# Kernel optimization log

Hardware: AMD Instinct MI355X
Metric: run time of the kernel (lower is better)

Reference implementation:

```python
import jax, jax.numpy as jnp
import numpy as np
import math

H = 4096; NH = 32; QLR = 1536; KVLR = 512
DN = 128; DR = 64; DV = 128; QD = DN + DR  # q_head_dim = 192
B = 1; S = 2048
BASE = 50000.0; FACTOR = 32.0; ORIG_MAX = 4096; BETA_FAST = 32.0; BETA_SLOW = 1.0
EPS = 1e-6
_M = 0.1 * 1.0 * math.log(FACTOR) + 1.0  # yarn mscale (mscale_all_dim=1)
SCALE = (QD ** -0.5) * _M * _M


def _yarn_cos_sin(seq_len):
    dim = DR
    f = np.arange(0, dim, 2, dtype=np.float32) / dim
    freq_extra = 1.0 / BASE ** f
    freq_inter = 1.0 / (FACTOR * BASE ** f)
    def corr(nr):
        return dim * math.log(ORIG_MAX / (nr * 2 * math.pi)) / (2 * math.log(BASE))
    low = max(math.floor(corr(BETA_FAST)), 0)
    high = min(math.ceil(corr(BETA_SLOW)), dim - 1)
    hi = high + 0.001 if low == high else float(high)
    ramp = np.clip((np.arange(dim // 2, dtype=np.float32) - low) / (hi - low), 0.0, 1.0)
    inv_freq_mask = 1.0 - ramp
    inv_freq = freq_inter * (1.0 - inv_freq_mask) + freq_extra * inv_freq_mask
    t = np.arange(seq_len, dtype=np.float32)
    fr = np.outer(t, inv_freq)
    emb = np.concatenate([fr, fr], axis=-1)
    # mscale ratio = get_mscale(f,1)/get_mscale(f,1) = 1.0
    return jnp.asarray(np.cos(emb)), jnp.asarray(np.sin(emb))


def _rms(x, w):
    v = jnp.mean(x.astype(jnp.float32) ** 2, axis=-1, keepdims=True)
    return w * (x.astype(jnp.float32) * jax.lax.rsqrt(v + EPS)).astype(x.dtype)


def _reorder(x):
    # interleaved -> [evens, odds] (matches view(d//2,2).transpose.reshape)
    d = x.shape[-1]
    x = x.reshape(x.shape[:-1] + (d // 2, 2))
    return jnp.concatenate([x[..., 0], x[..., 1]], axis=-1)


def _rotate_half(x):
    h = x.shape[-1] // 2
    return jnp.concatenate([-x[..., h:], x[..., :h]], axis=-1)


def _rope(x, cos, sin):
    x = _reorder(x)
    return x * cos + _rotate_half(x) * sin


def setup_inputs() -> dict:
    key = jax.random.key(0)
    ks = jax.random.split(key, 6)
    hs = jax.random.normal(ks[0], (B, S, H), dtype=jnp.float32)
    causal = jnp.tril(jnp.ones((S, S), dtype=bool))
    mask = jnp.where(causal, 0.0, -1e9).astype(jnp.float32)[None, None]
    pos = jnp.broadcast_to(jnp.arange(S, dtype=jnp.int64 if jax.config.jax_enable_x64 else jnp.int32), (B, S))
    def w(k, shape, fan_in):
        return jax.random.normal(k, shape, dtype=jnp.float32) * (fan_in ** -0.5)
    return {
        "hidden_states": hs,
        "attention_mask": mask,
        "position_ids": pos,
        "q_a_w": w(ks[1], (QLR, H), H),
        "q_a_ln_w": jnp.ones((QLR,), jnp.float32),
        "q_b_w": w(ks[2], (NH * QD, QLR), QLR),
        "kv_a_w": w(ks[3], (KVLR + DR, H), H),
        "kv_a_ln_w": jnp.ones((KVLR,), jnp.float32),
        "kv_b_w": w(ks[4], (NH * (DN + DV), KVLR), KVLR),
        "o_w": w(ks[5], (H, NH * DV), NH * DV),
    }


def reference(hidden_states, attention_mask, position_ids, q_a_w, q_a_ln_w, q_b_w, kv_a_w, kv_a_ln_w, kv_b_w, o_w):
    b, s, _ = hidden_states.shape
    q = _rms(hidden_states @ q_a_w.T, q_a_ln_w) @ q_b_w.T
    q = q.reshape(b, s, NH, QD).transpose(0, 2, 1, 3)          # [b,h,s,192]
    q_nope, q_pe = q[..., :DN], q[..., DN:]
    ckv = hidden_states @ kv_a_w.T                              # [b,s,576]
    comp, k_pe = ckv[..., :KVLR], ckv[..., KVLR:]
    k_pe = k_pe.reshape(b, s, 1, DR).transpose(0, 2, 1, 3)      # [b,1,s,64]
    kv = (_rms(comp, kv_a_ln_w) @ kv_b_w.T).reshape(b, s, NH, DN + DV).transpose(0, 2, 1, 3)
    k_nope, v = kv[..., :DN], kv[..., DN:]
    cos, sin = _yarn_cos_sin(s)
    cos = cos[position_ids][:, None]                            # [b,1,s,64]
    sin = sin[position_ids][:, None]
    q_pe = _rope(q_pe, cos, sin)
    k_pe = _rope(k_pe, cos, sin)
    qs = jnp.concatenate([q_nope, q_pe], axis=-1)               # [b,h,s,192]
    ks = jnp.concatenate([k_nope, jnp.broadcast_to(k_pe, (b, NH, s, DR))], axis=-1)
    aw = jnp.einsum('bhqd,bhkd->bhqk', qs, ks) * SCALE
    aw = jax.nn.softmax((aw + attention_mask).astype(jnp.float32), axis=-1).astype(hidden_states.dtype)
    out = jnp.einsum('bhqk,bhkd->bhqd', aw, v)                  # [b,h,s,128]
    out = out.transpose(0, 2, 1, 3).reshape(b, s, NH * DV)
    return out @ o_w.T
```

## Files before the change

kernel.cpp:

```cpp
#include <hip/hip_runtime.h>
#include <hip/hip_fp16.h>

typedef _Float16 f16x8 __attribute__((ext_vector_type(8)));
typedef float f32x4 __attribute__((ext_vector_type(4)));

#define DEV __device__ __forceinline__

typedef const __attribute__((address_space(1))) void gvoid_t;
typedef __attribute__((address_space(3))) void lvoid_t;

DEV void gload16(const void* g, void* l) {
  __builtin_amdgcn_global_load_lds((gvoid_t*)g, (lvoid_t*)l, 16, 0, 0);
}

DEV f32x4 mfma16(f16x8 a, f16x8 b, f32x4 c) {
  return __builtin_amdgcn_mfma_f32_16x16x32_f16(a, b, c, 0, 0, 0);
}

__global__ __launch_bounds__(256) void cvt_kernel(const float* __restrict__ s,
                                                  __half* __restrict__ d, int n4) {
  int stride = gridDim.x * 256;
  for (int i = blockIdx.x * 256 + threadIdx.x; i < n4; i += stride) {
    float4 v = ((const float4*)s)[i];
    __align__(8) __half a[4] = {__float2half(v.x), __float2half(v.y),
                                __float2half(v.z), __float2half(v.w)};
    *((uint2*)(d + (size_t)i * 4)) = *((uint2*)a);
  }
}

__global__ __launch_bounds__(256) void cvt5_kernel(const float* __restrict__ s0,
                                                   const float* __restrict__ s1,
                                                   const float* __restrict__ s2,
                                                   const float* __restrict__ s3,
                                                   const float* __restrict__ s4,
                                                   __half* __restrict__ d0, __half* __restrict__ d1,
                                                   __half* __restrict__ d2, __half* __restrict__ d3,
                                                   __half* __restrict__ d4) {
  const int c0 = 2097152, c1 = 3670016, c2 = 4259840, c3 = 6619136, c4 = 7667712;
  int stride = gridDim.x * 256;
  for (int i = blockIdx.x * 256 + threadIdx.x; i < c4; i += stride) {
    const float* s;
    __half* d;
    int j;
    if (i < c0) { s = s0; d = d0; j = i; }
    else if (i < c1) { s = s1; d = d1; j = i - c0; }
    else if (i < c2) { s = s2; d = d2; j = i - c1; }
    else if (i < c3) { s = s3; d = d3; j = i - c2; }
    else { s = s4; d = d4; j = i - c3; }
    float4 v = ((const float4*)s)[j];
    __align__(8) __half a[4] = {__float2half(v.x), __float2half(v.y),
                                __float2half(v.z), __float2half(v.w)};
    *((uint2*)(d + (size_t)j * 4)) = *((uint2*)a);
  }
}

__global__ __launch_bounds__(256) void norm_rope_kernel(const float* __restrict__ qab,
                                                        const float* __restrict__ q_ln,
                                                        const float* __restrict__ kv_ln,
                                                        const float2* __restrict__ cs,
                                                        __half* __restrict__ qa_r,
                                                        __half* __restrict__ kv_r,
                                                        __half* __restrict__ Kb) {
  const int row = blockIdx.x, tid = threadIdx.x;
  const float* xr = qab + (size_t)row * 2112;
  float4 a0 = ((const float4*)xr)[tid];
  float4 a1 = make_float4(0.f, 0.f, 0.f, 0.f);
  float4 b0 = make_float4(0.f, 0.f, 0.f, 0.f);
  if (tid < 128) {
    a1 = ((const float4*)xr)[256 + tid];
    b0 = ((const float4*)(xr + 1536))[tid];
  }
  float sq = a0.x * a0.x + a0.y * a0.y + a0.z * a0.z + a0.w * a0.w +
             a1.x * a1.x + a1.y * a1.y + a1.z * a1.z + a1.w * a1.w;
  float sk = b0.x * b0.x + b0.y * b0.y + b0.z * b0.z + b0.w * b0.w;
  for (int mm = 1; mm <= 32; mm <<= 1) {
    sq += __shfl_xor(sq, mm);
    sk += __shfl_xor(sk, mm);
  }
  __shared__ float r1[4], r2[4];
  __shared__ __half ro[64];
  if ((tid & 63) == 0) { r1[tid >> 6] = sq; r2[tid >> 6] = sk; }
  if (tid < 32) {
    float x0 = xr[2048 + 2 * tid], x1 = xr[2048 + 2 * tid + 1];
    float2 c = cs[row * 32 + tid];
    ro[tid] = __float2half(x0 * c.x - x1 * c.y);
    ro[32 + tid] = __float2half(x1 * c.x + x0 * c.y);
  }
  __syncthreads();
  float rsq = rsqrtf((r1[0] + r1[1] + r1[2] + r1[3]) * (1.f / 1536.f) + 1e-6f);
  float rsk = rsqrtf((r2[0] + r2[1] + r2[2] + r2[3]) * (1.f / 512.f) + 1e-6f);
  __half* yq = qa_r + (size_t)row * 1536;
  {
    int j = tid * 4;
    yq[j + 0] = __float2half(q_ln[j + 0] * a0.x * rsq);
    yq[j + 1] = __float2half(q_ln[j + 1] * a0.y * rsq);
    yq[j + 2] = __float2half(q_ln[j + 2] * a0.z * rsq);
    yq[j + 3] = __float2half(q_ln[j + 3] * a0.w * rsq);
  }
  if (tid < 128) {
    int j = 1024 + tid * 4;
    yq[j + 0] = __float2half(q_ln[j + 0] * a1.x * rsq);
    yq[j + 1] = __float2half(q_ln[j + 1] * a1.y * rsq);
    yq[j + 2] = __float2half(q_ln[j + 2] * a1.z * rsq);
    yq[j + 3] = __float2half(q_ln[j + 3] * a1.w * rsq);
    __half* yk = kv_r + (size_t)row * 512;
    int jk = tid * 4;
    yk[jk + 0] = __float2half(kv_ln[jk + 0] * b0.x * rsk);
    yk[jk + 1] = __float2half(kv_ln[jk + 1] * b0.y * rsk);
    yk[jk + 2] = __float2half(kv_ln[jk + 2] * b0.z * rsk);
    yk[jk + 3] = __float2half(kv_ln[jk + 3] * b0.w * rsk);
  }
#pragma unroll
  for (int it = 0; it < 8; ++it) {
    int i = it * 256 + tid;
    int hh = i >> 6, d = i & 63;
    Kb[((size_t)hh * 2048 + row) * 192 + 128 + d] = ro[d];
  }
}

__global__ __launch_bounds__(256) void rope_table_kernel(const int* __restrict__ pos,
                                                         float2* __restrict__ cs) {
  int i = blockIdx.x * 256 + threadIdx.x;
  int row = i >> 5, j = i & 31;
  double f = (double)j * (1.0 / 32.0);
  double fe = exp(-f * 10.81977828441028);
  double fi = fe * (1.0 / 32.0);
  double ramp = fmin(fmax(((double)j - 8.0) * (1.0 / 12.0), 0.0), 1.0);
  double inv = fi * ramp + fe * (1.0 - ramp);
  double ang = (double)pos[row] * inv;
  cs[i] = make_float2((float)cos(ang), (float)sin(ang));
}

__global__ __launch_bounds__(256) void rope_q_kernel(const __half* __restrict__ qpe,
                                                     const float2* __restrict__ cs,
                                                     __half* __restrict__ Qb, float qscale) {
  int i = blockIdx.x * 256 + threadIdx.x;
  int row = i >> 10, rem = i & 1023, h = rem >> 5, j = rem & 31;
  float x0 = __half2float(qpe[(size_t)row * 2048 + h * 64 + 2 * j]);
  float x1 = __half2float(qpe[(size_t)row * 2048 + h * 64 + 2 * j + 1]);
  float2 c = cs[row * 32 + j];
  float o0 = (x0 * c.x - x1 * c.y) * qscale;
  float o1 = (x1 * c.x + x0 * c.y) * qscale;
  __half* dst = Qb + ((size_t)h * 2048 + row) * 192;
  dst[128 + j] = __float2half(o0);
  dst[160 + j] = __float2half(o1);
}

template <int BN, int EPI>
__global__ __launch_bounds__(256) void gemm128(const __half* __restrict__ A, int lda,
                                               const __half* __restrict__ B, int K, int Ncols,
                                               float* __restrict__ Cf, int ldc,
                                               __half* __restrict__ O1, __half* __restrict__ O2,
                                               float qscale) {
  constexpr int NFR = BN / 32;
  __shared__ __align__(16) char As[2 * 128 * 128];
  __shared__ __align__(16) char Bs[2 * BN * 128];
  const int tid = threadIdx.x;
  const int lane = tid & 63, w = tid >> 6;
  const int l15 = lane & 15, g = lane >> 4;
  const int wr = w >> 1, wc = w & 1;
  const int nwg = gridDim.x * gridDim.y;
  int wg = blockIdx.y * gridDim.x + blockIdx.x;
  wg = (wg & 7) * (nwg >> 3) + (wg >> 3);
  const int m0 = (wg / gridDim.x) * 128, n0 = (wg % gridDim.x) * BN;
  const int srow = lane >> 3;
  const int scol = ((lane & 7) ^ srow) * 8;
  f32x4 acc[4][NFR] = {};
  const int nt = K >> 6;

  auto stage = [&](int t, int buf) {
    const __half* Ab = A + t * 64 + scol;
    const __half* Bb = B + t * 64 + scol;
#pragma unroll
    for (int cc = 0; cc < 4; ++cc) {
      int ch = w * 4 + cc;
      gload16(Ab + (size_t)(m0 + ch * 8 + srow) * lda, As + buf * 16384 + ch * 1024);
    }
#pragma unroll
    for (int cc = 0; cc < NFR; ++cc) {
      int ch = w * NFR + cc;
      gload16(Bb + (size_t)(n0 + ch * 8 + srow) * K, Bs + buf * (BN * 128) + ch * 1024);
    }
  };

  stage(0, 0);
  __syncthreads();

  for (int t = 0; t < nt; ++t) {
    const int buf = t & 1;
    if (t + 1 < nt) stage(t + 1, buf ^ 1);
    const char* Ab = As + buf * 16384;
    const char* Bb = Bs + buf * (BN * 128);
#pragma unroll
    for (int kk = 0; kk < 2; ++kk) {
      f16x8 af[4], bf[NFR];
#pragma unroll
      for (int m = 0; m < 4; ++m) {
        int r = wr * 64 + m * 16 + l15;
        af[m] = *(const f16x8*)(Ab + r * 128 + (((kk << 2) | g) ^ (r & 7)) * 16);
      }
#pragma unroll
      for (int n = 0; n < NFR; ++n) {
        int r = wc * (BN / 2) + n * 16 + l15;
        bf[n] = *(const f16x8*)(Bb + r * 128 + (((kk << 2) | g) ^ (r & 7)) * 16);
      }
#pragma unroll
      for (int m = 0; m < 4; ++m)
#pragma unroll
        for (int n = 0; n < NFR; ++n) acc[m][n] = mfma16(af[m], bf[n], acc[m][n]);
    }
    __syncthreads();
  }

#pragma unroll
  for (int m = 0; m < 4; ++m)
#pragma unroll
    for (int n = 0; n < NFR; ++n)
#pragma unroll
      for (int i = 0; i < 4; ++i) {
        int row = m0 + wr * 64 + m * 16 + g * 4 + i;
        int col = n0 + wc * (BN / 2) + n * 16 + l15;
        float v = acc[m][n][i];
        if (EPI == 0) {
          if (col < Ncols) Cf[(size_t)row * ldc + col] = v;
        } else if (EPI == 2) {
          int h = col / 192, d = col - h * 192;
          if (d < 128)
            O1[((size_t)h * 2048 + row) * 192 + d] = __float2half(v * qscale);
          else
            O2[(size_t)row * 2048 + h * 64 + (d - 128)] = __float2half(v);
        } else if (EPI == 3) {
          int h = col >> 8, d = col & 255;
          if (d < 128)
            O1[((size_t)h * 2048 + row) * 192 + d] = __float2half(v);
          else
            O2[((size_t)h * 128 + (d - 128)) * 2048 + row] = __float2half(v);
        }
      }
}

__global__ __launch_bounds__(256) void attn_kernel(const __half* __restrict__ Q,
                                                   const __half* __restrict__ K,
                                                   const __half* __restrict__ Vt,
                                                   __half* __restrict__ Out) {
  __shared__ __align__(16) char Klds[2 * 64 * 384];
  __shared__ __align__(16) char Vlds[144 * 128];
  __shared__ __align__(16) __half Plds[4][16][72];
  int wg = blockIdx.y * gridDim.x + blockIdx.x;
  wg = (wg & 7) * 64 + (wg >> 3);
  const int pr = wg & 15, h = wg >> 4;
  const int tid = threadIdx.x, lane = tid & 63, w = tid >> 6;
  const int l15 = lane & 15, g = lane >> 4;

  const char* Kg = (const char*)(K + (size_t)h * 2048 * 192);
  const char* Vg = (const char*)(Vt + (size_t)h * 128 * 2048);

  if (tid < 128) {
    ((uint4*)(Vlds + 16384))[tid] =
        make_uint4(0x3C003C00u, 0x3C003C00u, 0x3C003C00u, 0x3C003C00u);
  }

  int kL[6], kRow[6], kSS[6];
#pragma unroll
  for (int cc = 0; cc < 6; ++cc) {
    int c = w * 6 + cc;
    int L = c * 64 + lane;
    int row = (L * 2731) >> 16;
    int slot = L - row * 24;
    kL[cc] = c;
    kRow[cc] = row;
    kSS[cc] = (slot & ~7) | ((slot ^ row) & 7);
  }

  for (int ht = 0; ht < 2; ++ht) {
    const int qt = ht ? (31 - pr) : pr;
    const int q0 = qt * 64;
    const int nt = qt + 1;

    const __half* Qh = Q + ((size_t)h * 2048 + q0 + w * 16 + l15) * 192;
    f16x8 qf[6];
#pragma unroll
    for (int kc = 0; kc < 6; ++kc) qf[kc] = *(const f16x8*)(Qh + kc * 32 + g * 8);

    f32x4 acc[9] = {};
    float m_i[4];
#pragma unroll
    for (int i = 0; i < 4; ++i) m_i[i] = -1e30f;

#pragma unroll
    for (int cc = 0; cc < 6; ++cc)
      gload16(Kg + (size_t)kRow[cc] * 384 + kSS[cc] * 16, Klds + kL[cc] * 1024);
    __syncthreads();

    for (int t = 0; t < nt; ++t) {
      const int kv0 = t * 64;
      const char* Kcur = Klds + (t & 1) * 24576;

#pragma unroll
      for (int cc = 0; cc < 4; ++cc) {
        int c = w * 4 + cc;
        int L = c * 64 + lane;
        int d = L >> 3, slot = L & 7;
        int ss = slot ^ (d & 7);
        gload16(Vg + ((size_t)d * 2048 + kv0) * 2 + ss * 16, Vlds + c * 1024);
      }
      if (t + 1 < nt) {
        char* Knxt = Klds + ((t + 1) & 1) * 24576;
#pragma unroll
        for (int cc = 0; cc < 6; ++cc)
          gload16(Kg + (size_t)(kv0 + 64 + kRow[cc]) * 384 + kSS[cc] * 16,
                  Knxt + kL[cc] * 1024);
      }

      f32x4 s[4] = {};
#pragma unroll
      for (int kc = 0; kc < 6; ++kc) {
#pragma unroll
        for (int n = 0; n < 4; ++n) {
          int krow = n * 16 + l15;
          int slot = kc * 4 + g;
          int ss = (slot & ~7) | ((slot ^ krow) & 7);
          f16x8 kf = *(const f16x8*)(Kcur + krow * 384 + ss * 16);
          s[n] = mfma16(qf[kc], kf, s[n]);
        }
      }

      const bool diag = (t == nt - 1);
      float ps[4][4];
      float mt[4] = {-1e30f, -1e30f, -1e30f, -1e30f};
#pragma unroll
      for (int n = 0; n < 4; ++n)
#pragma unroll
        for (int i = 0; i < 4; ++i) {
          float v = s[n][i];
          if (diag) {
            int key = n * 16 + l15, qq = w * 16 + g * 4 + i;
            if (key > qq) v = -1e30f;
          }
          ps[n][i] = v;
          mt[i] = fmaxf(mt[i], v);
        }
#pragma unroll
      for (int mm = 1; mm <= 8; mm <<= 1)
#pragma unroll
        for (int i = 0; i < 4; ++i) mt[i] = fmaxf(mt[i], __shfl_xor(mt[i], mm));

      bool ok = true;
      float nm[4];
#pragma unroll
      for (int i = 0; i < 4; ++i) {
        nm[i] = fmaxf(m_i[i], mt[i]);
        ok = ok && (mt[i] - m_i[i] <= 8.0f);
      }
      if (!__all(ok)) {
#pragma unroll
        for (int i = 0; i < 4; ++i) {
          float c = exp2f(m_i[i] - nm[i]);
          m_i[i] = nm[i];
#pragma unroll
          for (int db = 0; db < 9; ++db) acc[db][i] *= c;
        }
      }
#pragma unroll
      for (int n = 0; n < 4; ++n)
#pragma unroll
        for (int i = 0; i < 4; ++i)
          Plds[w][g * 4 + i][n * 16 + l15] = __float2half(exp2f(ps[n][i] - m_i[i]));

      __syncthreads();

#pragma unroll
      for (int ks = 0; ks < 2; ++ks) {
        f16x8 pa = *(const f16x8*)((const char*)&Plds[w][0][0] + l15 * 144 + ks * 64 + g * 16);
#pragma unroll
        for (int db = 0; db < 9; ++db) {
          int d = db * 16 + l15;
          int ss = (ks * 4 + g) ^ (d & 7);
          f16x8 vf = *(const f16x8*)(Vlds + d * 128 + ss * 16);
          acc[db] = mfma16(pa, vf, acc[db]);
        }
      }
      __syncthreads();
    }

#pragma unroll
    for (int i = 0; i < 4; ++i) {
      float inv = 1.0f / acc[8][i];
#pragma unroll
      for (int db = 0; db < 8; ++db) {
        int row = q0 + w * 16 + g * 4 + i;
        Out[(size_t)row * 4096 + h * 128 + db * 16 + l15] = __float2half(acc[db][i] * inv);
      }
    }
  }
}

extern "C" void kernel_launch(void* const* d_in, const int* in_sizes, int n_in,
                              void* d_out, int out_size, void* d_ws, size_t ws_size,
                              hipStream_t stream) {
  (void)in_sizes; (void)n_in; (void)out_size; (void)ws_size;
  const float* hs = (const float*)d_in[0];
  const int* pos = (const int*)d_in[2];
  const float* q_a_w = (const float*)d_in[3];
  const float* q_a_ln = (const float*)d_in[4];
  const float* q_b_w = (const float*)d_in[5];
  const float* kv_a_w = (const float*)d_in[6];
  const float* kv_a_ln = (const float*)d_in[7];
  const float* kv_b_w = (const float*)d_in[8];
  const float* o_w = (const float*)d_in[9];

  char* p = (char*)d_ws;
  auto alloc = [&](size_t sz) { char* r = p; p += (sz + 255) & ~(size_t)255; return r; };
  __half* hs_h = (__half*)alloc((size_t)2048 * 4096 * 2);
  __half* w_qab = (__half*)alloc((size_t)2176 * 4096 * 2);
  __half* w_qb = (__half*)alloc((size_t)6144 * 1536 * 2);
  __half* w_kvb = (__half*)alloc((size_t)8192 * 512 * 2);
  float* qab_f = (float*)alloc((size_t)2048 * 2112 * 4);
  __half* qa_r = (__half*)alloc((size_t)2048 * 1536 * 2);
  __half* kv_r = (__half*)alloc((size_t)2048 * 512 * 2);
  float2* cs_tab = (float2*)alloc((size_t)2048 * 32 * 8);
  __half* Qb = (__half*)alloc((size_t)32 * 2048 * 192 * 2);
  __half* Kb = (__half*)alloc((size_t)32 * 2048 * 192 * 2);
  __half* Vtb = (__half*)alloc((size_t)32 * 128 * 2048 * 2);
  __half* qpe = (__half*)alloc((size_t)2048 * 2048 * 2);
  __half* attn_h = hs_h;
  __half* w_o = Qb;

  constexpr float QSCALE = 0.13086090981960297f * 1.4426950408889634f;

  cvt5_kernel<<<2048, 256, 0, stream>>>(hs, q_a_w, kv_a_w, q_b_w, kv_b_w,
                                        hs_h, w_qab, w_qab + (size_t)1536 * 4096,
                                        w_qb, w_kvb);
  rope_table_kernel<<<(2048 * 32) / 256, 256, 0, stream>>>(pos, cs_tab);

  gemm128<192, 0><<<dim3(11, 16), 256, 0, stream>>>(hs_h, 4096, w_qab, 4096, 2112, qab_f,
                                                    2112, nullptr, nullptr, 1.f);
  norm_rope_kernel<<<2048, 256, 0, stream>>>(qab_f, q_a_ln, kv_a_ln, cs_tab,
                                             qa_r, kv_r, Kb);
  gemm128<128, 2><<<dim3(48, 16), 256, 0, stream>>>(qa_r, 1536, w_qb, 1536, 6144, nullptr,
                                                    0, Qb, qpe, QSCALE);
  rope_q_kernel<<<(2048 * 1024) / 256, 256, 0, stream>>>(qpe, cs_tab, Qb, QSCALE);
  gemm128<128, 3><<<dim3(64, 16), 256, 0, stream>>>(kv_r, 512, w_kvb, 512, 8192, nullptr,
                                                    0, Kb, Vtb, 1.f);
  attn_kernel<<<dim3(16, 32), 256, 0, stream>>>(Qb, Kb, Vtb, attn_h);
  cvt_kernel<<<2048, 256, 0, stream>>>(o_w, w_o, (int)((size_t)4096 * 4096 / 4));
  gemm128<128, 0><<<dim3(32, 16), 256, 0, stream>>>(attn_h, 4096, w_o, 4096, 4096,
                                                    (float*)d_out, 4096, nullptr, nullptr,
                                                    1.f);
}
```

Before: 421.1 us.

## Rewrite attention with 32x32 MFMA, transposed scores, register P, and double-buffered V

The attention kernel now computes transposed scores S^T = K·Q^T with 32x32x16 MFMAs, so each lane owns one query row. The probabilities then stay in registers and are exchanged across half-waves with shuffles instead of going through an LDS buffer. V is double-buffered in LDS next to K, and the row sum is tracked explicitly instead of through a ones-column in V. Each workgroup now handles one 128-row query tile instead of a balanced pair of 64-row tiles, which removes the extra P sync but may cost load balance. It also raises register pressure, with launch bounds requesting 2 blocks per SIMD unit.

After: 436.5 us. +3.7%, slower.

```diff
diff --git a/kernel.cpp b/kernel.cpp
--- a/kernel.cpp
+++ b/kernel.cpp
@@ -3,6 +3,7 @@
 
 typedef _Float16 f16x8 __attribute__((ext_vector_type(8)));
 typedef float f32x4 __attribute__((ext_vector_type(4)));
+typedef float f32x16 __attribute__((ext_vector_type(16)));
 
 #define DEV __device__ __forceinline__
 
@@ -15,6 +16,10 @@
 
 DEV f32x4 mfma16(f16x8 a, f16x8 b, f32x4 c) {
   return __builtin_amdgcn_mfma_f32_16x16x32_f16(a, b, c, 0, 0, 0);
+}
+
+DEV f32x16 mfma32(f16x8 a, f16x8 b, f32x16 c) {
+  return __builtin_amdgcn_mfma_f32_32x32x16_f16(a, b, c, 0, 0, 0);
 }
 
 __global__ __launch_bounds__(256) void cvt_kernel(const float* __restrict__ s,
@@ -239,160 +244,165 @@
       }
 }
 
-__global__ __launch_bounds__(256) void attn_kernel(const __half* __restrict__ Q,
-                                                   const __half* __restrict__ K,
-                                                   const __half* __restrict__ Vt,
-                                                   __half* __restrict__ Out) {
+__global__ __launch_bounds__(256, 2) void attn_kernel(const __half* __restrict__ Q,
+                                                      const __half* __restrict__ K,
+                                                      const __half* __restrict__ Vt,
+                                                      __half* __restrict__ Out) {
   __shared__ __align__(16) char Klds[2 * 64 * 384];
-  __shared__ __align__(16) char Vlds[144 * 128];
-  __shared__ __align__(16) __half Plds[4][16][72];
+  __shared__ __align__(16) char Vlds[2 * 128 * 128];
   int wg = blockIdx.y * gridDim.x + blockIdx.x;
   wg = (wg & 7) * 64 + (wg >> 3);
-  const int pr = wg & 15, h = wg >> 4;
+  const int h = wg >> 4, qt = 15 - (wg & 15);
+  const int q0 = qt * 128;
+  const int nt = 2 * qt + 2;
   const int tid = threadIdx.x, lane = tid & 63, w = tid >> 6;
-  const int l15 = lane & 15, g = lane >> 4;
+  const int l31 = lane & 31, hf = lane >> 5;
+  const int qrow = q0 + w * 32 + l31;
+  const int maskT = (w < 2) ? nt - 2 : nt - 1;
 
   const char* Kg = (const char*)(K + (size_t)h * 2048 * 192);
   const char* Vg = (const char*)(Vt + (size_t)h * 128 * 2048);
 
-  if (tid < 128) {
-    ((uint4*)(Vlds + 16384))[tid] =
-        make_uint4(0x3C003C00u, 0x3C003C00u, 0x3C003C00u, 0x3C003C00u);
-  }
-
-  int kL[6], kRow[6], kSS[6];
+  int kRow[6], kSS[6];
 #pragma unroll
   for (int cc = 0; cc < 6; ++cc) {
     int c = w * 6 + cc;
     int L = c * 64 + lane;
     int row = (L * 2731) >> 16;
     int slot = L - row * 24;
-    kL[cc] = c;
     kRow[cc] = row;
     kSS[cc] = (slot & ~7) | ((slot ^ row) & 7);
   }
-
-  for (int ht = 0; ht < 2; ++ht) {
-    const int qt = ht ? (31 - pr) : pr;
-    const int q0 = qt * 64;
-    const int nt = qt + 1;
-
-    const __half* Qh = Q + ((size_t)h * 2048 + q0 + w * 16 + l15) * 192;
-    f16x8 qf[6];
-#pragma unroll
-    for (int kc = 0; kc < 6; ++kc) qf[kc] = *(const f16x8*)(Qh + kc * 32 + g * 8);
-
-    f32x4 acc[9] = {};
-    float m_i[4];
-#pragma unroll
-    for (int i = 0; i < 4; ++i) m_i[i] = -1e30f;
-
-#pragma unroll
-    for (int cc = 0; cc < 6; ++cc)
-      gload16(Kg + (size_t)kRow[cc] * 384 + kSS[cc] * 16, Klds + kL[cc] * 1024);
+  int vD[4], vSS[4];
+#pragma unroll
+  for (int cc = 0; cc < 4; ++cc) {
+    int c = w * 4 + cc;
+    int L = c * 64 + lane;
+    int d = L >> 3, slot = L & 7;
+    vD[cc] = d;
+    vSS[cc] = slot ^ (d & 7);
+  }
+
+  const __half* Qh = Q + ((size_t)h * 2048 + qrow) * 192;
+  f16x8 qf[12];
+#pragma unroll
+  for (int dblk = 0; dblk < 12; ++dblk)
+    qf[dblk] = *(const f16x8*)(Qh + dblk * 16 + hf * 8);
+
+  f32x16 acc[4] = {};
+  float m_i = -1e30f, l_i = 0.f;
+
+#pragma unroll
+  for (int cc = 0; cc < 6; ++cc)
+    gload16(Kg + (size_t)kRow[cc] * 384 + kSS[cc] * 16, Klds + (w * 6 + cc) * 1024);
+#pragma unroll
+  for (int cc = 0; cc < 4; ++cc)
+    gload16(Vg + ((size_t)vD[cc] * 2048) * 2 + vSS[cc] * 16, Vlds + (w * 4 + cc) * 1024);
+  __syncthreads();
+
+  for (int t = 0; t < nt; ++t) {
+    const int kv0 = t * 64;
+    if (t + 1 < nt) {
+      char* Kn = Klds + ((t + 1) & 1) * 24576;
+      char* Vn = Vlds + ((t + 1) & 1) * 16384;
+#pragma unroll
+      for (int cc = 0; cc < 6; ++cc)
+        gload16(Kg + (size_t)(kv0 + 64 + kRow[cc]) * 384 + kSS[cc] * 16,
+                Kn + (w * 6 + cc) * 1024);
+#pragma unroll
+      for (int cc = 0; cc < 4; ++cc)
+        gload16(Vg + ((size_t)vD[cc] * 2048 + kv0 + 64) * 2 + vSS[cc] * 16,
+                Vn + (w * 4 + cc) * 1024);
+    }
+
+    if (t <= maskT) {
+      const char* Kc = Klds + (t & 1) * 24576;
+      const char* Vc = Vlds + (t & 1) * 16384;
+      f32x16 sT0 = {}, sT1 = {};
+#pragma unroll
+      for (int dblk = 0; dblk < 12; ++dblk) {
+        int row0 = l31, slot = dblk * 2 + hf;
+        int ss0 = (slot & ~7) | ((slot ^ row0) & 7);
+        f16x8 kf0 = *(const f16x8*)(Kc + row0 * 384 + ss0 * 16);
+        sT0 = mfma32(kf0, qf[dblk], sT0);
+        int row1 = 32 + l31;
+        int ss1 = (slot & ~7) | ((slot ^ row1) & 7);
+        f16x8 kf1 = *(const f16x8*)(Kc + row1 * 384 + ss1 * 16);
+        sT1 = mfma32(kf1, qf[dblk], sT1);
+      }
+      float ps[32];
+#pragma unroll
+      for (int r = 0; r < 16; ++r) { ps[r] = sT0[r]; ps[16 + r] = sT1[r]; }
+      if (t == maskT) {
+#pragma unroll
+        for (int kb = 0; kb < 2; ++kb)
+#pragma unroll
+          for (int r = 0; r < 16; ++r) {
+            int kg = kv0 + kb * 32 + (r & 3) + 8 * (r >> 2) + 4 * hf;
+            if (kg > qrow) ps[kb * 16 + r] = -1e30f;
+          }
+      }
+      float mt = ps[0];
+#pragma unroll
+      for (int r = 1; r < 32; ++r) mt = fmaxf(mt, ps[r]);
+      mt = fmaxf(mt, __shfl_xor(mt, 32));
+      float nm = fmaxf(m_i, mt);
+      if (__any(mt - m_i > 8.f)) {
+        float corr = exp2f(m_i - nm);
+        m_i = nm;
+        l_i *= corr;
+#pragma unroll
+        for (int nb = 0; nb < 4; ++nb)
+#pragma unroll
+          for (int r = 0; r < 16; ++r) acc[nb][r] *= corr;
+      }
+      float rs = 0.f;
+      unsigned pk[16];
+#pragma unroll
+      for (int r = 0; r < 16; ++r) {
+        float pa = exp2f(ps[2 * r] - m_i);
+        float pb = exp2f(ps[2 * r + 1] - m_i);
+        rs += pa + pb;
+        __half2 hh = __floats2half2_rn(pa, pb);
+        pk[r] = *(unsigned*)&hh;
+      }
+      rs += __shfl_xor(rs, 32);
+      l_i += rs;
+#pragma unroll
+      for (int ks = 0; ks < 4; ++ks) {
+        int base = (ks >> 1) * 8 + (ks & 1) * 4;
+        unsigned q0u = pk[base + 0], q1u = pk[base + 1];
+        unsigned q2u = pk[base + 2], q3u = pk[base + 3];
+        unsigned s0 = __shfl_xor(q0u, 32), s1 = __shfl_xor(q1u, 32);
+        unsigned s2 = __shfl_xor(q2u, 32), s3 = __shfl_xor(q3u, 32);
+        union { f16x8 v; unsigned u[4]; } pb_;
+        pb_.u[0] = hf ? s2 : q0u;
+        pb_.u[1] = hf ? s3 : q1u;
+        pb_.u[2] = hf ? q2u : s0;
+        pb_.u[3] = hf ? q3u : s1;
+#pragma unroll
+        for (int nb = 0; nb < 4; ++nb) {
+          int d = nb * 32 + l31;
+          int ss = (ks * 2 + hf) ^ (d & 7);
+          f16x8 vf = *(const f16x8*)(Vc + d * 128 + ss * 16);
+          acc[nb] = mfma32(vf, pb_.v, acc[nb]);
+        }
+      }
+    }
     __syncthreads();
-
-    for (int t = 0; t < nt; ++t) {
-      const int kv0 = t * 64;
-      const char* Kcur = Klds + (t & 1) * 24576;
-
-#pragma unroll
-      for (int cc = 0; cc < 4; ++cc) {
-        int c = w * 4 + cc;
-        int L = c * 64 + lane;
-        int d = L >> 3, slot = L & 7;
-        int ss = slot ^ (d & 7);
-        gload16(Vg + ((size_t)d * 2048 + kv0) * 2 + ss * 16, Vlds + c * 1024);
-      }
-      if (t + 1 < nt) {
-        char* Knxt = Klds + ((t + 1) & 1) * 24576;
-#pragma unroll
-        for (int cc = 0; cc < 6; ++cc)
-          gload16(Kg + (size_t)(kv0 + 64 + kRow[cc]) * 384 + kSS[cc] * 16,
-                  Knxt + kL[cc] * 1024);
-      }
-
-      f32x4 s[4] = {};
-#pragma unroll
-      for (int kc = 0; kc < 6; ++kc) {
-#pragma unroll
-        for (int n = 0; n < 4; ++n) {
-          int krow = n * 16 + l15;
-          int slot = kc * 4 + g;
-          int ss = (slot & ~7) | ((slot ^ krow) & 7);
-          f16x8 kf = *(const f16x8*)(Kcur + krow * 384 + ss * 16);
-          s[n] = mfma16(qf[kc], kf, s[n]);
-        }
-      }
-
-      const bool diag = (t == nt - 1);
-      float ps[4][4];
-      float mt[4] = {-1e30f, -1e30f, -1e30f, -1e30f};
-#pragma unroll
-      for (int n = 0; n < 4; ++n)
-#pragma unroll
-        for (int i = 0; i < 4; ++i) {
-          float v = s[n][i];
-          if (diag) {
-            int key = n * 16 + l15, qq = w * 16 + g * 4 + i;
-            if (key > qq) v = -1e30f;
-          }
-          ps[n][i] = v;
-          mt[i] = fmaxf(mt[i], v);
-        }
-#pragma unroll
-      for (int mm = 1; mm <= 8; mm <<= 1)
-#pragma unroll
-        for (int i = 0; i < 4; ++i) mt[i] = fmaxf(mt[i], __shfl_xor(mt[i], mm));
-
-      bool ok = true;
-      float nm[4];
-#pragma unroll
-      for (int i = 0; i < 4; ++i) {
-        nm[i] = fmaxf(m_i[i], mt[i]);
-        ok = ok && (mt[i] - m_i[i] <= 8.0f);
-      }
-      if (!__all(ok)) {
-#pragma unroll
-        for (int i = 0; i < 4; ++i) {
-          float c = exp2f(m_i[i] - nm[i]);
-          m_i[i] = nm[i];
-#pragma unroll
-          for (int db = 0; db < 9; ++db) acc[db][i] *= c;
-        }
-      }
-#pragma unroll
-      for (int n = 0; n < 4; ++n)
-#pragma unroll
-        for (int i = 0; i < 4; ++i)
-          Plds[w][g * 4 + i][n * 16 + l15] = __float2half(exp2f(ps[n][i] - m_i[i]));
-
-      __syncthreads();
-
-#pragma unroll
-      for (int ks = 0; ks < 2; ++ks) {
-        f16x8 pa = *(const f16x8*)((const char*)&Plds[w][0][0] + l15 * 144 + ks * 64 + g * 16);
-#pragma unroll
-        for (int db = 0; db < 9; ++db) {
-          int d = db * 16 + l15;
-          int ss = (ks * 4 + g) ^ (d & 7);
-          f16x8 vf = *(const f16x8*)(Vlds + d * 128 + ss * 16);
-          acc[db] = mfma16(pa, vf, acc[db]);
-        }
-      }
-      __syncthreads();
-    }
-
-#pragma unroll
-    for (int i = 0; i < 4; ++i) {
-      float inv = 1.0f / acc[8][i];
-#pragma unroll
-      for (int db = 0; db < 8; ++db) {
-        int row = q0 + w * 16 + g * 4 + i;
-        Out[(size_t)row * 4096 + h * 128 + db * 16 + l15] = __float2half(acc[db][i] * inv);
-      }
-    }
-  }
+  }
+
+  float inv = 1.0f / l_i;
+  __half* Or = Out + (size_t)qrow * 4096 + h * 128;
+#pragma unroll
+  for (int nb = 0; nb < 4; ++nb)
+#pragma unroll
+    for (int r2 = 0; r2 < 4; ++r2) {
+      __align__(8) __half h4[4];
+#pragma unroll
+      for (int j = 0; j < 4; ++j) h4[j] = __float2half(acc[nb][r2 * 4 + j] * inv);
+      *(uint2*)(Or + nb * 32 + r2 * 8 + hf * 4) = *(uint2*)h4;
+    }
 }
 
 extern "C" void kernel_launch(void* const* d_in, const int* in_sizes, int n_in,
```
